# Optimization experiments

Hardware: AMD Instinct MI355X
Metric: run time of the kernel (lower is better)

## Reference

```python
import jax, jax.numpy as jnp
import numpy as np

D_DEC = 256  # decoder_size; W columns are [decoder | encoder] per the torch concat order


def setup_inputs() -> dict:
    key = jax.random.key(0)
    k1, k2, k3, k4 = jax.random.split(key, 4)
    B, S, E, D, A = 32, 4096, 256, 256, 256
    decoder_hidden = jax.random.normal(k1, (1, B, D), dtype=jnp.float32)
    encoder_outputs = jax.random.normal(k2, (S, B, E), dtype=jnp.float32)
    W = jax.random.normal(k3, (A, D + E), dtype=jnp.float32) / np.sqrt(D + E)
    b = jax.random.normal(k4, (A,), dtype=jnp.float32) * 0.02
    return {"decoder_hidden": decoder_hidden, "encoder_outputs": encoder_outputs, "W": W, "b": b}


def reference(decoder_hidden, encoder_outputs, W, b):
    # decoder_hidden: [1,B,D] -> [B,D]; encoder_outputs: [S,B,E] -> [B,S,E]
    dh = decoder_hidden[0]
    eo = jnp.transpose(encoder_outputs, (1, 0, 2))
    # Split the concat-linear: cat([dec, enc]) @ W.T == dec @ Wd.T + enc @ We.T
    Wd, We = W[:, :D_DEC], W[:, D_DEC:]
    # scores: tanh(linear) summed over attn dim -> [B,S]
    proj = dh @ Wd.T + b  # [B,A]
    attn = jnp.tanh(proj[:, None, :] + jnp.einsum('bse,ae->bsa', eo, We))
    scores = jnp.sum(attn, axis=2)  # [B,S]
    attn_softmax = jax.nn.softmax(scores, axis=1)  # [B,S]
    attended = jnp.einsum('bs,bse->be', attn_softmax, eo)  # [B,E]
    encoder_norms = jnp.linalg.norm(eo, axis=2)  # [B,S]
    attn_map = attn_softmax * encoder_norms
    return attended, attn_map
```

## Files before the change

### kernel.cpp

```cpp
#include <hip/hip_runtime.h>
#include <math.h>

#define B_  32
#define S_  4096
#define E_  256
#define A_  256
#define DE_ 512

typedef __attribute__((ext_vector_type(8))) short short8;
typedef __attribute__((ext_vector_type(4))) float f32x4;

__device__ inline unsigned short f2bf(float x) {
    unsigned int u = __float_as_uint(x);
    u += 0x7FFFu + ((u >> 16) & 1u);
    return (unsigned short)(u >> 16);
}
__device__ inline float tanh_fast(float x) {
    x = fminf(fmaxf(x, -15.f), 15.f);
    float t = __expf(2.f * x);
    return (t - 1.f) * __builtin_amdgcn_rcpf(t + 1.f);
}

__device__ __forceinline__ void conv_write(float4 v0, float4 v1,
                                           unsigned short* buf, int eu,
                                           float& nacc)
{
    nacc += v0.x*v0.x + v0.y*v0.y + v0.z*v0.z + v0.w*v0.w
          + v1.x*v1.x + v1.y*v1.y + v1.z*v1.z + v1.w*v1.w;
    float xs[8] = {v0.x, v0.y, v0.z, v0.w, v1.x, v1.y, v1.z, v1.w};
    unsigned int hp[4], lp[4];
    #pragma unroll
    for (int j = 0; j < 4; ++j) {
        unsigned int u0 = __float_as_uint(xs[2*j])   & 0xFFFF0000u;
        unsigned int u1 = __float_as_uint(xs[2*j+1]) & 0xFFFF0000u;
        hp[j] = (u0 >> 16) | u1;
        lp[j] = (unsigned int)f2bf(xs[2*j]   - __uint_as_float(u0))
              | ((unsigned int)f2bf(xs[2*j+1] - __uint_as_float(u1)) << 16);
    }
    *(uint4*)&buf[(size_t)eu * 8]         = make_uint4(hp[0], hp[1], hp[2], hp[3]);
    *(uint4*)&buf[(size_t)(264 + eu) * 8] = make_uint4(lp[0], lp[1], lp[2], lp[3]);
}

__global__ __launch_bounds__(256) void prep_kernel(
    const float* __restrict__ W, const float* __restrict__ dh,
    const float* __restrict__ bias, unsigned short* __restrict__ wepk,
    float* __restrict__ proj, float* __restrict__ out)
{
    __shared__ float dh_lds[E_];
    const int bk  = blockIdx.x;
    const int tid = threadIdx.x;
    if (bk < 64) {
        const int idx = bk * 256 + tid;
        const int c     = idx >> 11;
        const int r     = idx & 2047;
        const int plane = r >> 10;
        const int kg    = (r >> 8) & 3;
        const int a     = r & 255;
        const float* src = W + (size_t)a * DE_ + E_ + c * 32 + kg * 8;
        unsigned int pk[4];
        #pragma unroll
        for (int j = 0; j < 4; ++j) {
            float x0 = src[2 * j], x1 = src[2 * j + 1];
            unsigned int u0 = __float_as_uint(x0) & 0xFFFF0000u;
            unsigned int u1 = __float_as_uint(x1) & 0xFFFF0000u;
            if (plane) {
                unsigned short l0 = f2bf(x0 - __uint_as_float(u0));
                unsigned short l1 = f2bf(x1 - __uint_as_float(u1));
                pk[j] = (unsigned int)l0 | ((unsigned int)l1 << 16);
            } else {
                pk[j] = (u0 >> 16) | u1;
            }
        }
        *(uint4*)&wepk[(size_t)idx * 8] = make_uint4(pk[0], pk[1], pk[2], pk[3]);
    } else if (bk < 96) {
        const int b = bk - 64;
        const int a = tid;
        dh_lds[a] = dh[b * E_ + a];
        __syncthreads();
        float acc = bias[a];
        const float* wrow = W + (size_t)a * DE_;
        #pragma unroll
        for (int d = 0; d < E_; d += 4) {
            float4 w = *(const float4*)(wrow + d);
            acc += dh_lds[d] * w.x + dh_lds[d+1] * w.y
                 + dh_lds[d+2] * w.z + dh_lds[d+3] * w.w;
        }
        proj[b * A_ + a] = acc;
    } else {
        #pragma unroll
        for (int j = tid; j < B_ * E_; j += 256) out[j] = 0.f;
    }
}

__global__ __launch_bounds__(256, 3) void scores_kernel(
    const float* __restrict__ eo, const unsigned short* __restrict__ wepk,
    const float* __restrict__ proj,
    float* __restrict__ scores, float* __restrict__ nsq)
{
    __shared__ __align__(16) unsigned char pool[18944];
    unsigned short* eo_hl = (unsigned short*)pool;

    const int tid = threadIdx.x;
    const int b   = blockIdx.x & (B_ - 1);
    const int s0  = (blockIdx.x >> 5) * 64;
    const int w   = tid >> 6, l = tid & 63;
    const int lq  = l >> 4,  lr = l & 15;

    const int erow = tid >> 2;
    const int ekg  = tid & 3;
    const float* ebase = eo + (size_t)(s0 + erow) * (B_ * E_) + b * E_ + ekg * 8;
    const int eu = ekg * 66 + erow;

    const int wunit = lq * 256 + w * 64 + lr;

    f32x4 acc[4][4];
    #pragma unroll
    for (int i = 0; i < 4; ++i)
        #pragma unroll
        for (int j = 0; j < 4; ++j)
            acc[i][j] = (f32x4){0.f, 0.f, 0.f, 0.f};
    float nacc = 0.f;

    float pr[4];
    #pragma unroll
    for (int nt = 0; nt < 4; ++nt) pr[nt] = proj[b * A_ + w * 64 + nt * 16 + lr];

    {
        float4 v0 = *(const float4*)(ebase);
        float4 v1 = *(const float4*)(ebase + 4);
        conv_write(v0, v1, eo_hl, eu, nacc);
    }
    float4 va0 = *(const float4*)(ebase + 32);
    float4 va1 = *(const float4*)(ebase + 36);
    __syncthreads();

    for (int c = 0; c < 8; ++c) {
        const int p = c & 1;
        unsigned short* rb = eo_hl + (size_t)p * 528 * 8;
        unsigned short* wb = eo_hl + (size_t)(1 - p) * 528 * 8;

        short8 bh[4], bl[4];
        {
            const unsigned short* wsrc = wepk + (size_t)(c * 2048 + wunit) * 8;
            #pragma unroll
            for (int nt = 0; nt < 4; ++nt) {
                bh[nt] = *(const short8*)(wsrc + (size_t)(nt * 16) * 8);
                bl[nt] = *(const short8*)(wsrc + (size_t)(1024 + nt * 16) * 8);
            }
        }
        short8 ah[2], al[2];
        #pragma unroll
        for (int mt = 0; mt < 2; ++mt) {
            const int au = lq * 66 + mt * 16 + lr;
            ah[mt] = *(const short8*)&rb[(size_t)au * 8];
            al[mt] = *(const short8*)&rb[(size_t)(264 + au) * 8];
        }
        if (c < 7) conv_write(va0, va1, wb, eu, nacc);
        if (c < 6) {
            va0 = *(const float4*)(ebase + (c + 2) * 32);
            va1 = *(const float4*)(ebase + (c + 2) * 32 + 4);
        }
        #pragma unroll
        for (int mt = 0; mt < 2; ++mt) {
            #pragma unroll
            for (int nt = 0; nt < 4; ++nt) {
                acc[mt][nt] = __builtin_amdgcn_mfma_f32_16x16x32_bf16(ah[mt], bh[nt], acc[mt][nt], 0, 0, 0);
                acc[mt][nt] = __builtin_amdgcn_mfma_f32_16x16x32_bf16(ah[mt], bl[nt], acc[mt][nt], 0, 0, 0);
                acc[mt][nt] = __builtin_amdgcn_mfma_f32_16x16x32_bf16(al[mt], bh[nt], acc[mt][nt], 0, 0, 0);
            }
        }
        #pragma unroll
        for (int mt = 2; mt < 4; ++mt) {
            const int au = lq * 66 + mt * 16 + lr;
            short8 ah2 = *(const short8*)&rb[(size_t)au * 8];
            short8 al2 = *(const short8*)&rb[(size_t)(264 + au) * 8];
            #pragma unroll
            for (int nt = 0; nt < 4; ++nt) {
                acc[mt][nt] = __builtin_amdgcn_mfma_f32_16x16x32_bf16(ah2, bh[nt], acc[mt][nt], 0, 0, 0);
                acc[mt][nt] = __builtin_amdgcn_mfma_f32_16x16x32_bf16(ah2, bl[nt], acc[mt][nt], 0, 0, 0);
                acc[mt][nt] = __builtin_amdgcn_mfma_f32_16x16x32_bf16(al2, bh[nt], acc[mt][nt], 0, 0, 0);
            }
        }
        if (c < 7) __syncthreads();
    }
    __syncthreads();

    float* red4  = (float*)pool;
    float* npart = (float*)(pool + 16896);
    float* qpart = (float*)(pool + 17920);
    #pragma unroll
    for (int mt = 0; mt < 4; ++mt) {
        #pragma unroll
        for (int r = 0; r < 4; ++r) {
            float s = 0.f;
            #pragma unroll
            for (int nt = 0; nt < 4; ++nt)
                s += tanh_fast(pr[nt] + acc[mt][nt][r]);
            red4[(w * 16 + lr) * 66 + (mt * 16 + lq * 4 + r)] = s;
        }
    }
    npart[tid] = nacc;
    __syncthreads();
    {
        const int row = tid >> 2, quarter = tid & 3;
        float s = 0.f;
        #pragma unroll
        for (int j = 0; j < 16; ++j) s += red4[(quarter * 16 + j) * 66 + row];
        qpart[quarter * 64 + row] = s;
    }
    __syncthreads();
    if (tid < 64) {
        scores[b * S_ + s0 + tid] = qpart[tid] + qpart[64 + tid]
                                  + qpart[128 + tid] + qpart[192 + tid];
        nsq[b * S_ + s0 + tid] = npart[4 * tid] + npart[4 * tid + 1]
                               + npart[4 * tid + 2] + npart[4 * tid + 3];
    }
}

__global__ __launch_bounds__(256) void stats_kernel(
    const float* __restrict__ scores, float* __restrict__ nsq_pv,
    float* __restrict__ out)
{
    __shared__ float red[256];
    const int tid  = threadIdx.x;
    const int b    = blockIdx.x & (B_ - 1);
    const int part = blockIdx.x >> 5;
    float v[16];
    float m = -1e30f;
    #pragma unroll
    for (int i = 0; i < 16; ++i) {
        v[i] = scores[b * S_ + i * 256 + tid];
        m = fmaxf(m, v[i]);
    }
    red[tid] = m;
    __syncthreads();
    for (int off = 128; off > 0; off >>= 1) {
        if (tid < off) red[tid] = fmaxf(red[tid], red[tid + off]);
        __syncthreads();
    }
    m = red[0];
    __syncthreads();
    float sum = 0.f;
    #pragma unroll
    for (int i = 0; i < 16; ++i) sum += __expf(v[i] - m);
    red[tid] = sum;
    __syncthreads();
    for (int off = 128; off > 0; off >>= 1) {
        if (tid < off) red[tid] += red[tid + off];
        __syncthreads();
    }
    const float inv = 1.f / red[0];
    #pragma unroll
    for (int j = 0; j < 2; ++j) {
        const int i = part * 2 + j;
        const int s = i * 256 + tid;
        const float pv = __expf(v[i] - m) * inv;
        out[B_ * E_ + b * S_ + s] = pv * sqrtf(nsq_pv[b * S_ + s]);
        nsq_pv[b * S_ + s] = pv;
    }
}

__global__ __launch_bounds__(256) void attend_kernel(
    const float* __restrict__ eo, const float* __restrict__ pv,
    float* __restrict__ out)
{
    __shared__ float4 acc_red[4][64];
    const int tid = threadIdx.x;
    const int b   = blockIdx.x & (B_ - 1);
    const int ch  = blockIdx.x / B_;
    const int le = tid & 63, sg = tid >> 6;
    const int s0 = ch * 128 + sg * 32;
    float4 a = make_float4(0.f, 0.f, 0.f, 0.f);
    #pragma unroll 8
    for (int s = 0; s < 32; ++s) {
        float p = pv[b * S_ + s0 + s];
        float4 e = *(const float4*)(eo + (size_t)(s0 + s) * (B_ * E_)
                                       + b * E_ + le * 4);
        a.x = fmaf(p, e.x, a.x);
        a.y = fmaf(p, e.y, a.y);
        a.z = fmaf(p, e.z, a.z);
        a.w = fmaf(p, e.w, a.w);
    }
    acc_red[sg][le] = a;
    __syncthreads();
    if (tid < 64) {
        float4 a0 = acc_red[0][tid], a1 = acc_red[1][tid];
        float4 a2 = acc_red[2][tid], a3 = acc_red[3][tid];
        float* dst = out + b * E_ + tid * 4;
        atomicAdd(dst + 0, a0.x + a1.x + a2.x + a3.x);
        atomicAdd(dst + 1, a0.y + a1.y + a2.y + a3.y);
        atomicAdd(dst + 2, a0.z + a1.z + a2.z + a3.z);
        atomicAdd(dst + 3, a0.w + a1.w + a2.w + a3.w);
    }
}

extern "C" void kernel_launch(void* const* d_in, const int* in_sizes, int n_in,
                              void* d_out, int out_size, void* d_ws, size_t ws_size,
                              hipStream_t stream)
{
    const float* dh   = (const float*)d_in[0];
    const float* eo   = (const float*)d_in[1];
    const float* W    = (const float*)d_in[2];
    const float* bias = (const float*)d_in[3];
    float* out = (float*)d_out;
    float* ws  = (float*)d_ws;

    float* projb  = ws;
    float* nsqb   = ws + 8192;
    float* scores = nsqb + S_ * B_;
    unsigned short* wepk = (unsigned short*)(scores + S_ * B_);

    prep_kernel   <<<97,              256, 0, stream>>>(W, dh, bias, wepk, projb, out);
    scores_kernel <<<B_ * (S_ / 64),  256, 0, stream>>>(eo, wepk, projb, scores, nsqb);
    stats_kernel  <<<B_ * 8,          256, 0, stream>>>(scores, nsqb, out);
    attend_kernel <<<B_ * (S_ / 128), 256, 0, stream>>>(eo, nsqb, out);
}
```

Baseline: 259.6 us.

## Quad-buffer encoder tiles in LDS and halve barriers in scores kernel

The scores kernel's K loop moves from double buffering with one barrier per 32-wide chunk to four LDS buffers processed two chunks per iteration. That halves the barrier count and keeps two global loads in flight per thread. MFMA sections are bracketed with s_setprio to favor the matrix issue, and barriers become a raw lgkmcnt wait plus s_barrier. LDS per block grows from about 19KB to 33KB, which may limit occupancy, and the extra prefetch registers raise register pressure under launch_bounds(256,3).

```diff
diff --git a/kernel.cpp b/kernel.cpp
--- a/kernel.cpp
+++ b/kernel.cpp
@@ -97,7 +97,7 @@
     const float* __restrict__ proj,
     float* __restrict__ scores, float* __restrict__ nsq)
 {
-    __shared__ __align__(16) unsigned char pool[18944];
+    __shared__ __align__(16) unsigned char pool[33792];
     unsigned short* eo_hl = (unsigned short*)pool;
 
     const int tid = threadIdx.x;
@@ -129,59 +129,114 @@
         float4 v0 = *(const float4*)(ebase);
         float4 v1 = *(const float4*)(ebase + 4);
         conv_write(v0, v1, eo_hl, eu, nacc);
-    }
-    float4 va0 = *(const float4*)(ebase + 32);
-    float4 va1 = *(const float4*)(ebase + 36);
-    __syncthreads();
-
-    for (int c = 0; c < 8; ++c) {
-        const int p = c & 1;
-        unsigned short* rb = eo_hl + (size_t)p * 528 * 8;
-        unsigned short* wb = eo_hl + (size_t)(1 - p) * 528 * 8;
-
-        short8 bh[4], bl[4];
+        float4 v2 = *(const float4*)(ebase + 32);
+        float4 v3 = *(const float4*)(ebase + 36);
+        conv_write(v2, v3, eo_hl + (size_t)528 * 8, eu, nacc);
+    }
+    float4 vaA0 = *(const float4*)(ebase + 64);
+    float4 vaA1 = *(const float4*)(ebase + 68);
+    float4 vaB0 = *(const float4*)(ebase + 96);
+    float4 vaB1 = *(const float4*)(ebase + 100);
+    asm volatile("s_waitcnt lgkmcnt(0)\ns_barrier" ::: "memory");
+
+    for (int p = 0; p < 4; ++p) {
+        const int c0 = 2 * p, c1 = 2 * p + 1;
+        unsigned short* rb0 = eo_hl + (size_t)(c0 & 3) * 528 * 8;
+        unsigned short* rb1 = eo_hl + (size_t)(c1 & 3) * 528 * 8;
+        unsigned short* wb0 = eo_hl + (size_t)((c0 + 2) & 3) * 528 * 8;
+        unsigned short* wb1 = eo_hl + (size_t)((c1 + 2) & 3) * 528 * 8;
+
         {
-            const unsigned short* wsrc = wepk + (size_t)(c * 2048 + wunit) * 8;
+            short8 bh[4], bl[4];
+            const unsigned short* wsrc = wepk + (size_t)(c0 * 2048 + wunit) * 8;
             #pragma unroll
             for (int nt = 0; nt < 4; ++nt) {
                 bh[nt] = *(const short8*)(wsrc + (size_t)(nt * 16) * 8);
                 bl[nt] = *(const short8*)(wsrc + (size_t)(1024 + nt * 16) * 8);
             }
-        }
-        short8 ah[2], al[2];
-        #pragma unroll
-        for (int mt = 0; mt < 2; ++mt) {
-            const int au = lq * 66 + mt * 16 + lr;
-            ah[mt] = *(const short8*)&rb[(size_t)au * 8];
-            al[mt] = *(const short8*)&rb[(size_t)(264 + au) * 8];
-        }
-        if (c < 7) conv_write(va0, va1, wb, eu, nacc);
-        if (c < 6) {
-            va0 = *(const float4*)(ebase + (c + 2) * 32);
-            va1 = *(const float4*)(ebase + (c + 2) * 32 + 4);
-        }
-        #pragma unroll
-        for (int mt = 0; mt < 2; ++mt) {
+            short8 ah[2], al[2];
+            #pragma unroll
+            for (int mt = 0; mt < 2; ++mt) {
+                const int au = lq * 66 + mt * 16 + lr;
+                ah[mt] = *(const short8*)&rb0[(size_t)au * 8];
+                al[mt] = *(const short8*)&rb0[(size_t)(264 + au) * 8];
+            }
+            if (p < 3) conv_write(vaA0, vaA1, wb0, eu, nacc);
+            __builtin_amdgcn_s_setprio(1);
+            #pragma unroll
+            for (int mt = 0; mt < 2; ++mt) {
+                #pragma unroll
+                for (int nt = 0; nt < 4; ++nt) {
+                    acc[mt][nt] = __builtin_amdgcn_mfma_f32_16x16x32_bf16(ah[mt], bh[nt], acc[mt][nt], 0, 0, 0);
+                    acc[mt][nt] = __builtin_amdgcn_mfma_f32_16x16x32_bf16(ah[mt], bl[nt], acc[mt][nt], 0, 0, 0);
+                    acc[mt][nt] = __builtin_amdgcn_mfma_f32_16x16x32_bf16(al[mt], bh[nt], acc[mt][nt], 0, 0, 0);
+                }
+            }
+            __builtin_amdgcn_s_setprio(0);
+            #pragma unroll
+            for (int mt = 2; mt < 4; ++mt) {
+                const int au = lq * 66 + mt * 16 + lr;
+                short8 ah2 = *(const short8*)&rb0[(size_t)au * 8];
+                short8 al2 = *(const short8*)&rb0[(size_t)(264 + au) * 8];
+                __builtin_amdgcn_s_setprio(1);
+                #pragma unroll
+                for (int nt = 0; nt < 4; ++nt) {
+                    acc[mt][nt] = __builtin_amdgcn_mfma_f32_16x16x32_bf16(ah2, bh[nt], acc[mt][nt], 0, 0, 0);
+                    acc[mt][nt] = __builtin_amdgcn_mfma_f32_16x16x32_bf16(ah2, bl[nt], acc[mt][nt], 0, 0, 0);
+                    acc[mt][nt] = __builtin_amdgcn_mfma_f32_16x16x32_bf16(al2, bh[nt], acc[mt][nt], 0, 0, 0);
+                }
+                __builtin_amdgcn_s_setprio(0);
+            }
+        }
+        {
+            short8 bh[4], bl[4];
+            const unsigned short* wsrc = wepk + (size_t)(c1 * 2048 + wunit) * 8;
             #pragma unroll
             for (int nt = 0; nt < 4; ++nt) {
-                acc[mt][nt] = __builtin_amdgcn_mfma_f32_16x16x32_bf16(ah[mt], bh[nt], acc[mt][nt], 0, 0, 0);
-                acc[mt][nt] = __builtin_amdgcn_mfma_f32_16x16x32_bf16(ah[mt], bl[nt], acc[mt][nt], 0, 0, 0);
-                acc[mt][nt] = __builtin_amdgcn_mfma_f32_16x16x32_bf16(al[mt], bh[nt], acc[mt][nt], 0, 0, 0);
-            }
-        }
-        #pragma unroll
-        for (int mt = 2; mt < 4; ++mt) {
-            const int au = lq * 66 + mt * 16 + lr;
-            short8 ah2 = *(const short8*)&rb[(size_t)au * 8];
-            short8 al2 = *(const short8*)&rb[(size_t)(264 + au) * 8];
-            #pragma unroll
-            for (int nt = 0; nt < 4; ++nt) {
-                acc[mt][nt] = __builtin_amdgcn_mfma_f32_16x16x32_bf16(ah2, bh[nt], acc[mt][nt], 0, 0, 0);
-                acc[mt][nt] = __builtin_amdgcn_mfma_f32_16x16x32_bf16(ah2, bl[nt], acc[mt][nt], 0, 0, 0);
-                acc[mt][nt] = __builtin_amdgcn_mfma_f32_16x16x32_bf16(al2, bh[nt], acc[mt][nt], 0, 0, 0);
-            }
-        }
-        if (c < 7) __syncthreads();
+                bh[nt] = *(const short8*)(wsrc + (size_t)(nt * 16) * 8);
+                bl[nt] = *(const short8*)(wsrc + (size_t)(1024 + nt * 16) * 8);
+            }
+            short8 ah[2], al[2];
+            #pragma unroll
+            for (int mt = 0; mt < 2; ++mt) {
+                const int au = lq * 66 + mt * 16 + lr;
+                ah[mt] = *(const short8*)&rb1[(size_t)au * 8];
+                al[mt] = *(const short8*)&rb1[(size_t)(264 + au) * 8];
+            }
+            if (p < 3) conv_write(vaB0, vaB1, wb1, eu, nacc);
+            __builtin_amdgcn_s_setprio(1);
+            #pragma unroll
+            for (int mt = 0; mt < 2; ++mt) {
+                #pragma unroll
+                for (int nt = 0; nt < 4; ++nt) {
+                    acc[mt][nt] = __builtin_amdgcn_mfma_f32_16x16x32_bf16(ah[mt], bh[nt], acc[mt][nt], 0, 0, 0);
+                    acc[mt][nt] = __builtin_amdgcn_mfma_f32_16x16x32_bf16(ah[mt], bl[nt], acc[mt][nt], 0, 0, 0);
+                    acc[mt][nt] = __builtin_amdgcn_mfma_f32_16x16x32_bf16(al[mt], bh[nt], acc[mt][nt], 0, 0, 0);
+                }
+            }
+            __builtin_amdgcn_s_setprio(0);
+            #pragma unroll
+            for (int mt = 2; mt < 4; ++mt) {
+                const int au = lq * 66 + mt * 16 + lr;
+                short8 ah2 = *(const short8*)&rb1[(size_t)au * 8];
+                short8 al2 = *(const short8*)&rb1[(size_t)(264 + au) * 8];
+                __builtin_amdgcn_s_setprio(1);
+                #pragma unroll
+                for (int nt = 0; nt < 4; ++nt) {
+                    acc[mt][nt] = __builtin_amdgcn_mfma_f32_16x16x32_bf16(ah2, bh[nt], acc[mt][nt], 0, 0, 0);
+                    acc[mt][nt] = __builtin_amdgcn_mfma_f32_16x16x32_bf16(ah2, bl[nt], acc[mt][nt], 0, 0, 0);
+                    acc[mt][nt] = __builtin_amdgcn_mfma_f32_16x16x32_bf16(al2, bh[nt], acc[mt][nt], 0, 0, 0);
+                }
+                __builtin_amdgcn_s_setprio(0);
+            }
+        }
+        if (p < 2) {
+            vaA0 = *(const float4*)(ebase + (2 * p + 4) * 32);
+            vaA1 = *(const float4*)(ebase + (2 * p + 4) * 32 + 4);
+            vaB0 = *(const float4*)(ebase + (2 * p + 5) * 32);
+            vaB1 = *(const float4*)(ebase + (2 * p + 5) * 32 + 4);
+        }
+        asm volatile("s_waitcnt lgkmcnt(0)\ns_barrier" ::: "memory");
     }
     __syncthreads();
 
```

Measured after the change: 254.3 us. 2.0% less time.

## Stream encoder tiles via global_load_lds into a 4-deep LDS ring

Applied to the files above, without the earlier changes.

Replaces register-staged prefetch of encoder rows with asynchronous global_load_lds DMA into a four-stage fp32 LDS ring buffer. The loads are meant to run further ahead than before and to ease register pressure. Each chunk is then converted to hi/lo bf16 from LDS into a single buffer, using hand-placed vmcnt waits and barriers. The low-part conversion also switches from round-to-nearest to truncation, trading a little accuracy for fewer ALU ops. LDS use rises to about 41KB, which may limit occupancy, and the extra barrier per chunk serializes conversion and MFMA.

```diff
diff --git a/kernel.cpp b/kernel.cpp
--- a/kernel.cpp
+++ b/kernel.cpp
@@ -10,6 +10,10 @@
 typedef __attribute__((ext_vector_type(8))) short short8;
 typedef __attribute__((ext_vector_type(4))) float f32x4;
 
+#define WAITV(n) asm volatile("s_waitcnt vmcnt(" #n ")" ::: "memory")
+#define LGKM0()  asm volatile("s_waitcnt lgkmcnt(0)" ::: "memory")
+#define BAR()    asm volatile("s_barrier" ::: "memory")
+
 __device__ inline unsigned short f2bf(float x) {
     unsigned int u = __float_as_uint(x);
     u += 0x7FFFu + ((u >> 16) & 1u);
@@ -34,8 +38,8 @@
         unsigned int u0 = __float_as_uint(xs[2*j])   & 0xFFFF0000u;
         unsigned int u1 = __float_as_uint(xs[2*j+1]) & 0xFFFF0000u;
         hp[j] = (u0 >> 16) | u1;
-        lp[j] = (unsigned int)f2bf(xs[2*j]   - __uint_as_float(u0))
-              | ((unsigned int)f2bf(xs[2*j+1] - __uint_as_float(u1)) << 16);
+        lp[j] = (__float_as_uint(xs[2*j]   - __uint_as_float(u0)) >> 16)
+              | ((__float_as_uint(xs[2*j+1] - __uint_as_float(u1)) >> 16) << 16);
     }
     *(uint4*)&buf[(size_t)eu * 8]         = make_uint4(hp[0], hp[1], hp[2], hp[3]);
     *(uint4*)&buf[(size_t)(264 + eu) * 8] = make_uint4(lp[0], lp[1], lp[2], lp[3]);
@@ -97,8 +101,9 @@
     const float* __restrict__ proj,
     float* __restrict__ scores, float* __restrict__ nsq)
 {
-    __shared__ __align__(16) unsigned char pool[18944];
-    unsigned short* eo_hl = (unsigned short*)pool;
+    __shared__ __align__(16) unsigned char pool[41216];
+    float*          fp32buf = (float*)pool;
+    unsigned short* bfbuf   = (unsigned short*)(pool + 32768);
 
     const int tid = threadIdx.x;
     const int b   = blockIdx.x & (B_ - 1);
@@ -106,10 +111,10 @@
     const int w   = tid >> 6, l = tid & 63;
     const int lq  = l >> 4,  lr = l & 15;
 
-    const int erow = tid >> 2;
-    const int ekg  = tid & 3;
-    const float* ebase = eo + (size_t)(s0 + erow) * (B_ * E_) + b * E_ + ekg * 8;
-    const int eu = ekg * 66 + erow;
+    const int ekg = l & 3;
+    const int eu  = ekg * 66 + (w * 16 + (l >> 2));
+    const float* gsrc = eo + (size_t)(s0 + w * 16 + (l >> 2)) * (B_ * E_)
+                           + b * E_ + ekg * 8;
 
     const int wunit = lq * 256 + w * 64 + lr;
 
@@ -125,20 +130,33 @@
     #pragma unroll
     for (int nt = 0; nt < 4; ++nt) pr[nt] = proj[b * A_ + w * 64 + nt * 16 + lr];
 
-    {
-        float4 v0 = *(const float4*)(ebase);
-        float4 v1 = *(const float4*)(ebase + 4);
-        conv_write(v0, v1, eo_hl, eu, nacc);
-    }
-    float4 va0 = *(const float4*)(ebase + 32);
-    float4 va1 = *(const float4*)(ebase + 36);
-    __syncthreads();
-
+    auto issue_dma = [&](int cc) {
+        #pragma unroll
+        for (int k = 0; k < 2; ++k) {
+            __builtin_amdgcn_global_load_lds(
+                (const __attribute__((address_space(1))) void*)(gsrc + cc * 32 + k * 4),
+                (__attribute__((address_space(3))) void*)&fp32buf[(cc & 3) * 2048 + w * 512 + k * 256],
+                16, 0, 0);
+        }
+    };
+
+    issue_dma(0); issue_dma(1); issue_dma(2); issue_dma(3);
+
+    #pragma unroll
     for (int c = 0; c < 8; ++c) {
-        const int p = c & 1;
-        unsigned short* rb = eo_hl + (size_t)p * 528 * 8;
-        unsigned short* wb = eo_hl + (size_t)(1 - p) * 528 * 8;
-
+        if      (c <= 4) WAITV(6);
+        else if (c == 5) WAITV(4);
+        else if (c == 6) WAITV(2);
+        else             WAITV(0);
+        BAR();
+        {
+            float4 v0 = *(const float4*)&fp32buf[(c & 3) * 2048 + w * 512 + l * 4];
+            float4 v1 = *(const float4*)&fp32buf[(c & 3) * 2048 + w * 512 + 256 + l * 4];
+            conv_write(v0, v1, bfbuf, eu, nacc);
+        }
+        LGKM0();
+        BAR();
+        if (c < 4) issue_dma(c + 4);
         short8 bh[4], bl[4];
         {
             const unsigned short* wsrc = wepk + (size_t)(c * 2048 + wunit) * 8;
@@ -152,13 +170,8 @@
         #pragma unroll
         for (int mt = 0; mt < 2; ++mt) {
             const int au = lq * 66 + mt * 16 + lr;
-            ah[mt] = *(const short8*)&rb[(size_t)au * 8];
-            al[mt] = *(const short8*)&rb[(size_t)(264 + au) * 8];
-        }
-        if (c < 7) conv_write(va0, va1, wb, eu, nacc);
-        if (c < 6) {
-            va0 = *(const float4*)(ebase + (c + 2) * 32);
-            va1 = *(const float4*)(ebase + (c + 2) * 32 + 4);
+            ah[mt] = *(const short8*)&bfbuf[(size_t)au * 8];
+            al[mt] = *(const short8*)&bfbuf[(size_t)(264 + au) * 8];
         }
         #pragma unroll
         for (int mt = 0; mt < 2; ++mt) {
@@ -172,8 +185,8 @@
         #pragma unroll
         for (int mt = 2; mt < 4; ++mt) {
             const int au = lq * 66 + mt * 16 + lr;
-            short8 ah2 = *(const short8*)&rb[(size_t)au * 8];
-            short8 al2 = *(const short8*)&rb[(size_t)(264 + au) * 8];
+            short8 ah2 = *(const short8*)&bfbuf[(size_t)au * 8];
+            short8 al2 = *(const short8*)&bfbuf[(size_t)(264 + au) * 8];
             #pragma unroll
             for (int nt = 0; nt < 4; ++nt) {
                 acc[mt][nt] = __builtin_amdgcn_mfma_f32_16x16x32_bf16(ah2, bh[nt], acc[mt][nt], 0, 0, 0);
@@ -181,7 +194,6 @@
                 acc[mt][nt] = __builtin_amdgcn_mfma_f32_16x16x32_bf16(al2, bh[nt], acc[mt][nt], 0, 0, 0);
             }
         }
-        if (c < 7) __syncthreads();
     }
     __syncthreads();
 
```

After: 257.9 us. Within noise of the previous version (-0.6%).

## Fuse attended reduction into scores kernel with per-block softmax partials

Applied to the files above, without the earlier changes.

The scores kernel now keeps a bf16 copy of its encoder tile in shared memory and computes a block-local softmax max, sum and weighted partial of the attended vector. A new combine kernel rescales and merges these partials per batch, replacing the separate attend kernel that re-read the full encoder tensor. This removes a second full pass over encoder_outputs and the atomics. In exchange it raises shared memory use per block, which may reduce occupancy, and computes the attended output from bf16-rounded encoder values.

```diff
diff --git a/kernel.cpp b/kernel.cpp
--- a/kernel.cpp
+++ b/kernel.cpp
@@ -23,12 +23,13 @@
 
 __device__ __forceinline__ void conv_write(float4 v0, float4 v1,
                                            unsigned short* buf, int eu,
+                                           unsigned short* rt,
                                            float& nacc)
 {
     nacc += v0.x*v0.x + v0.y*v0.y + v0.z*v0.z + v0.w*v0.w
           + v1.x*v1.x + v1.y*v1.y + v1.z*v1.z + v1.w*v1.w;
     float xs[8] = {v0.x, v0.y, v0.z, v0.w, v1.x, v1.y, v1.z, v1.w};
-    unsigned int hp[4], lp[4];
+    unsigned int hp[4], lp[4], rp[4];
     #pragma unroll
     for (int j = 0; j < 4; ++j) {
         unsigned int u0 = __float_as_uint(xs[2*j])   & 0xFFFF0000u;
@@ -36,15 +37,18 @@
         hp[j] = (u0 >> 16) | u1;
         lp[j] = (unsigned int)f2bf(xs[2*j]   - __uint_as_float(u0))
               | ((unsigned int)f2bf(xs[2*j+1] - __uint_as_float(u1)) << 16);
+        rp[j] = (unsigned int)f2bf(xs[2*j])
+              | ((unsigned int)f2bf(xs[2*j+1]) << 16);
     }
     *(uint4*)&buf[(size_t)eu * 8]         = make_uint4(hp[0], hp[1], hp[2], hp[3]);
     *(uint4*)&buf[(size_t)(264 + eu) * 8] = make_uint4(lp[0], lp[1], lp[2], lp[3]);
+    *(uint4*)&rt[(size_t)eu * 8]          = make_uint4(rp[0], rp[1], rp[2], rp[3]);
 }
 
 __global__ __launch_bounds__(256) void prep_kernel(
     const float* __restrict__ W, const float* __restrict__ dh,
     const float* __restrict__ bias, unsigned short* __restrict__ wepk,
-    float* __restrict__ proj, float* __restrict__ out)
+    float* __restrict__ proj)
 {
     __shared__ float dh_lds[E_];
     const int bk  = blockIdx.x;
@@ -72,7 +76,7 @@
             }
         }
         *(uint4*)&wepk[(size_t)idx * 8] = make_uint4(pk[0], pk[1], pk[2], pk[3]);
-    } else if (bk < 96) {
+    } else {
         const int b = bk - 64;
         const int a = tid;
         dh_lds[a] = dh[b * E_ + a];
@@ -86,19 +90,18 @@
                  + dh_lds[d+2] * w.z + dh_lds[d+3] * w.w;
         }
         proj[b * A_ + a] = acc;
-    } else {
-        #pragma unroll
-        for (int j = tid; j < B_ * E_; j += 256) out[j] = 0.f;
     }
 }
 
 __global__ __launch_bounds__(256, 3) void scores_kernel(
     const float* __restrict__ eo, const unsigned short* __restrict__ wepk,
     const float* __restrict__ proj,
-    float* __restrict__ scores, float* __restrict__ nsq)
-{
-    __shared__ __align__(16) unsigned char pool[18944];
-    unsigned short* eo_hl = (unsigned short*)pool;
+    float* __restrict__ scores, float* __restrict__ nsq,
+    float* __restrict__ Pbuf)
+{
+    __shared__ __align__(16) unsigned char pool[52736];
+    unsigned short* eo_hl  = (unsigned short*)pool;
+    unsigned short* retain = (unsigned short*)(pool + 18944);
 
     const int tid = threadIdx.x;
     const int b   = blockIdx.x & (B_ - 1);
@@ -128,7 +131,7 @@
     {
         float4 v0 = *(const float4*)(ebase);
         float4 v1 = *(const float4*)(ebase + 4);
-        conv_write(v0, v1, eo_hl, eu, nacc);
+        conv_write(v0, v1, eo_hl, eu, retain, nacc);
     }
     float4 va0 = *(const float4*)(ebase + 32);
     float4 va1 = *(const float4*)(ebase + 36);
@@ -155,7 +158,8 @@
             ah[mt] = *(const short8*)&rb[(size_t)au * 8];
             al[mt] = *(const short8*)&rb[(size_t)(264 + au) * 8];
         }
-        if (c < 7) conv_write(va0, va1, wb, eu, nacc);
+        if (c < 7) conv_write(va0, va1, wb, eu,
+                              retain + (size_t)(c + 1) * 264 * 8, nacc);
         if (c < 6) {
             va0 = *(const float4*)(ebase + (c + 2) * 32);
             va1 = *(const float4*)(ebase + (c + 2) * 32 + 4);
@@ -209,16 +213,42 @@
         qpart[quarter * 64 + row] = s;
     }
     __syncthreads();
+    float* ws = npart;
     if (tid < 64) {
-        scores[b * S_ + s0 + tid] = qpart[tid] + qpart[64 + tid]
-                                  + qpart[128 + tid] + qpart[192 + tid];
+        const float sc = qpart[tid] + qpart[64 + tid]
+                       + qpart[128 + tid] + qpart[192 + tid];
+        scores[b * S_ + s0 + tid] = sc;
         nsq[b * S_ + s0 + tid] = npart[4 * tid] + npart[4 * tid + 1]
                                + npart[4 * tid + 2] + npart[4 * tid + 3];
+        float mb = sc;
+        #pragma unroll
+        for (int off = 32; off > 0; off >>= 1)
+            mb = fmaxf(mb, __shfl_xor(mb, off, 64));
+        const float wv = __expf(sc - mb);
+        float zb = wv;
+        #pragma unroll
+        for (int off = 32; off > 0; off >>= 1)
+            zb += __shfl_xor(zb, off, 64);
+        ws[tid] = wv;
+        if (tid == 0) {
+            Pbuf[(size_t)blockIdx.x * 258 + 256] = mb;
+            Pbuf[(size_t)blockIdx.x * 258 + 257] = zb;
+        }
+    }
+    __syncthreads();
+    {
+        const int c2 = tid >> 5, kg2 = (tid >> 3) & 3, j2 = tid & 7;
+        const unsigned short* rt = retain + (size_t)(c2 * 264 + kg2 * 66) * 8 + j2;
+        float accp = 0.f;
+        #pragma unroll 8
+        for (int s = 0; s < 64; ++s)
+            accp += ws[s] * __uint_as_float((unsigned int)rt[(size_t)s * 8] << 16);
+        Pbuf[(size_t)blockIdx.x * 258 + tid] = accp;
     }
 }
 
 __global__ __launch_bounds__(256) void stats_kernel(
-    const float* __restrict__ scores, float* __restrict__ nsq_pv,
+    const float* __restrict__ scores, const float* __restrict__ nsq,
     float* __restrict__ out)
 {
     __shared__ float red[256];
@@ -255,43 +285,33 @@
         const int i = part * 2 + j;
         const int s = i * 256 + tid;
         const float pv = __expf(v[i] - m) * inv;
-        out[B_ * E_ + b * S_ + s] = pv * sqrtf(nsq_pv[b * S_ + s]);
-        nsq_pv[b * S_ + s] = pv;
-    }
-}
-
-__global__ __launch_bounds__(256) void attend_kernel(
-    const float* __restrict__ eo, const float* __restrict__ pv,
-    float* __restrict__ out)
-{
-    __shared__ float4 acc_red[4][64];
+        out[B_ * E_ + b * S_ + s] = pv * sqrtf(nsq[b * S_ + s]);
+    }
+}
+
+__global__ __launch_bounds__(256) void combine_kernel(
+    const float* __restrict__ Pbuf, float* __restrict__ out)
+{
+    __shared__ float mz[128];
+    __shared__ float sc[64];
     const int tid = threadIdx.x;
-    const int b   = blockIdx.x & (B_ - 1);
-    const int ch  = blockIdx.x / B_;
-    const int le = tid & 63, sg = tid >> 6;
-    const int s0 = ch * 128 + sg * 32;
-    float4 a = make_float4(0.f, 0.f, 0.f, 0.f);
+    const int b   = blockIdx.x;
+    if (tid < 64)       mz[tid] = Pbuf[(size_t)(tid * 32 + b) * 258 + 256];
+    else if (tid < 128) mz[tid] = Pbuf[(size_t)((tid - 64) * 32 + b) * 258 + 257];
+    __syncthreads();
+    float m = -1e30f;
+    #pragma unroll
+    for (int i = 0; i < 64; ++i) m = fmaxf(m, mz[i]);
+    float Z = 0.f;
+    #pragma unroll
+    for (int i = 0; i < 64; ++i) Z += mz[64 + i] * __expf(mz[i] - m);
+    if (tid < 64) sc[tid] = __expf(mz[tid] - m);
+    __syncthreads();
+    float acc = 0.f;
     #pragma unroll 8
-    for (int s = 0; s < 32; ++s) {
-        float p = pv[b * S_ + s0 + s];
-        float4 e = *(const float4*)(eo + (size_t)(s0 + s) * (B_ * E_)
-                                       + b * E_ + le * 4);
-        a.x = fmaf(p, e.x, a.x);
-        a.y = fmaf(p, e.y, a.y);
-        a.z = fmaf(p, e.z, a.z);
-        a.w = fmaf(p, e.w, a.w);
-    }
-    acc_red[sg][le] = a;
-    __syncthreads();
-    if (tid < 64) {
-        float4 a0 = acc_red[0][tid], a1 = acc_red[1][tid];
-        float4 a2 = acc_red[2][tid], a3 = acc_red[3][tid];
-        float* dst = out + b * E_ + tid * 4;
-        atomicAdd(dst + 0, a0.x + a1.x + a2.x + a3.x);
-        atomicAdd(dst + 1, a0.y + a1.y + a2.y + a3.y);
-        atomicAdd(dst + 2, a0.z + a1.z + a2.z + a3.z);
-        atomicAdd(dst + 3, a0.w + a1.w + a2.w + a3.w);
-    }
+    for (int blk = 0; blk < 64; ++blk)
+        acc += Pbuf[(size_t)(blk * 32 + b) * 258 + tid] * sc[blk];
+    out[b * E_ + tid] = acc / Z;
 }
 
 extern "C" void kernel_launch(void* const* d_in, const int* in_sizes, int n_in,
@@ -308,10 +328,11 @@
     float* projb  = ws;
     float* nsqb   = ws + 8192;
     float* scores = nsqb + S_ * B_;
-    unsigned short* wepk = (unsigned short*)(scores + S_ * B_);
-
-    prep_kernel   <<<97,              256, 0, stream>>>(W, dh, bias, wepk, projb, out);
-    scores_kernel <<<B_ * (S_ / 64),  256, 0, stream>>>(eo, wepk, projb, scores, nsqb);
-    stats_kernel  <<<B_ * 8,          256, 0, stream>>>(scores, nsqb, out);
-    attend_kernel <<<B_ * (S_ / 128), 256, 0, stream>>>(eo, nsqb, out);
-}
+    float* Pbuf   = scores + S_ * B_;
+    unsigned short* wepk = (unsigned short*)(Pbuf + 2048 * 258);
+
+    prep_kernel    <<<96,              256, 0, stream>>>(W, dh, bias, wepk, projb);
+    scores_kernel  <<<B_ * (S_ / 64),  256, 0, stream>>>(eo, wepk, projb, scores, nsqb, Pbuf);
+    stats_kernel   <<<B_ * 8,          256, 0, stream>>>(scores, nsqb, out);
+    combine_kernel <<<B_,              256, 0, stream>>>(Pbuf, out);
+}
```

Result: faster. 242.5 us, median of 2 (-6.6%).
